# Performance work log

Hardware: AMD Instinct MI355X
Metric: run time of the kernel (lower is better)

The kernel has to match this reference:

```python
import jax, jax.numpy as jnp
import numpy as np

B, L, D_IN, D_MODEL, D_OUT, N_LAYERS, N2 = 16, 2048, 512, 512, 512, 4, 32
Q_STEP = 1.0 / 64.0
LN_EPS = 1e-5


def setup_inputs() -> dict:
    key = jax.random.key(0)
    ks = jax.random.split(key, 12)
    H = D_MODEL
    x = jax.random.normal(ks[0], (B, D_IN, L), jnp.float32)
    # sigma-delta dense encoder / decoder weights (ANN-equivalent: dense + ReLU)
    W_enc = jax.random.normal(ks[1], (H, D_IN), jnp.float32) * (1.0 / np.sqrt(D_IN))
    W_dec = jax.random.normal(ks[2], (D_OUT, H), jnp.float32) * (1.0 / np.sqrt(H))
    # S4D kernel params, stacked over layers. S4D-Lin init.
    log_dt = (jax.random.uniform(ks[3], (N_LAYERS, H), jnp.float32)
              * (np.log(0.1) - np.log(0.001)) + np.log(0.001))
    log_A_real = jnp.full((N_LAYERS, H, N2), np.log(0.5), jnp.float32)
    A_imag = jnp.tile((np.pi * jnp.arange(N2, dtype=jnp.float32))[None, None, :],
                      (N_LAYERS, H, 1))
    C_re = jax.random.normal(ks[4], (N_LAYERS, H, N2), jnp.float32) * (0.5 ** 0.5)
    C_im = jax.random.normal(ks[5], (N_LAYERS, H, N2), jnp.float32) * (0.5 ** 0.5)
    D = jax.random.normal(ks[6], (N_LAYERS, H), jnp.float32)
    # output linear of each S4D block: 1x1 conv H -> 2H followed by GLU
    W_out = jax.random.normal(ks[7], (N_LAYERS, 2 * H, H), jnp.float32) * (1.0 / np.sqrt(H))
    b_out = jnp.zeros((N_LAYERS, 2 * H), jnp.float32)
    ln_g = jnp.ones((N_LAYERS, H), jnp.float32)
    ln_b = jnp.zeros((N_LAYERS, H), jnp.float32)
    return {"x": x, "W_enc": W_enc, "W_dec": W_dec, "log_dt": log_dt,
            "log_A_real": log_A_real, "A_imag": A_imag, "C_re": C_re,
            "C_im": C_im, "D": D, "W_out": W_out, "b_out": b_out,
            "ln_g": ln_g, "ln_b": ln_b}


def _quantize_ste(x, step):
    q = jnp.round(x / step) * step
    return x + jax.lax.stop_gradient(q - x)


def reference(x, W_enc, W_dec, log_dt, log_A_real, A_imag, C_re, C_im, D,
              W_out, b_out, ln_g, ln_b):
    # x: (B, d_input, L) channel-time layout (slayer convention)
    xq = _quantize_ste(x, Q_STEP)
    h = jax.nn.relu(jnp.einsum('bct,dc->bdt', xq, W_enc))  # encoder (B,H,L)
    Lx = h.shape[-1]
    t = jnp.arange(Lx)
    for i in range(N_LAYERS):
        # ---- S4D kernel (ZOH-style discretization) ----
        dt = jnp.exp(log_dt[i])[:, None]                 # (H,1)
        A = -jnp.exp(log_A_real[i]) + 1j * A_imag[i]     # (H,N)
        dtA = dt * A                                     # (H,N)
        Cc = (C_re[i] + 1j * C_im[i]) * jnp.expm1(dtA) / A
        vand = jnp.exp(dtA[:, :, None] * t)              # (H,N,L)
        K = 2.0 * jnp.einsum('hn,hnl->hl', Cc, vand).real  # (H,L)
        # ---- FFT convolution ----
        k_f = jnp.fft.rfft(K, n=2 * Lx)                  # (H, L+1)
        u_f = jnp.fft.rfft(h, n=2 * Lx)                  # (B,H,L+1)
        y = jnp.fft.irfft(u_f * k_f[None], n=2 * Lx)[..., :Lx]
        y = y + D[i][:, None] * h                        # skip connection
        y = jax.nn.gelu(y, approximate=False)
        # output linear: 1x1 conv H->2H + GLU over channel dim
        z = jnp.einsum('bht,dh->bdt', y, W_out[i]) + b_out[i][None, :, None]
        z = z[:, :D_MODEL] * jax.nn.sigmoid(z[:, D_MODEL:])
        # residual + post-norm (LayerNorm over channel dim)
        h = z + h
        mu = h.mean(axis=1, keepdims=True)
        var = h.var(axis=1, keepdims=True)
        h = (h - mu) / jnp.sqrt(var + LN_EPS) * ln_g[i][:, None] + ln_b[i][:, None]
    out = jax.nn.relu(jnp.einsum('bht,dh->bdt', h, W_dec))  # decoder (B,d_out,L)
    return out
```

## Files before the change

### kernel.cpp

```cpp
#include <hip/hip_runtime.h>
#include <cstdint>
#include <cstddef>

typedef __attribute__((ext_vector_type(8))) short short8;
typedef __attribute__((ext_vector_type(8))) _Float16 half8;
typedef __attribute__((ext_vector_type(4))) float floatx4;
typedef __attribute__((ext_vector_type(4))) int intx4;
typedef __attribute__((ext_vector_type(4))) unsigned short ushort4v;

__device__ __forceinline__ unsigned short f2h(float f) {
    union { _Float16 h; unsigned short u; } v;
    v.h = (_Float16)f;
    return v.u;
}
__device__ __forceinline__ float relu_keepnan(float v) {
    return v > 0.f ? v : (v == v ? 0.f : v);
}

__global__ __launch_bounds__(256) void k_cvt(
    const float* __restrict__ src, unsigned short* __restrict__ dst, int n) {
    int i = blockIdx.x * 256 + threadIdx.x;
    if (i < n) dst[i] = f2h(src[i]);
}

__global__ __launch_bounds__(256) void k_precompute(
    const float* __restrict__ ldt, const float* __restrict__ lar,
    const float* __restrict__ aim, const float* __restrict__ cre,
    const float* __restrict__ cim, float4* __restrict__ lwc,
    float2* __restrict__ wt) {
    int idx = blockIdx.x * 256 + threadIdx.x;
    int i = idx >> 14;
    int h = (idx >> 5) & 511;
    int n = idx & 31;
    float dt = expf(ldt[i * 512 + h]);
    float Are = -expf(lar[idx]);
    float Aim = aim[idx];
    float dre = dt * Are, dim = dt * Aim;
    float e = expf(dre);
    float wre = e * cosf(dim);
    float wim = e * sinf(dim);
    float emr = wre - 1.f, emi = wim;
    float inv = 1.f / (Are * Are + Aim * Aim);
    float fr = (emr * Are + emi * Aim) * inv;
    float fi = (emi * Are - emr * Aim) * inv;
    float cr = cre[idx], ci = cim[idx];
    float4 o;
    o.x = wre; o.y = wim;
    o.z = 2.f * (cr * fr - ci * fi);
    o.w = 2.f * (cr * fi + ci * fr);
    int oidx = (i * 32 + n) * 512 + h;
    lwc[oidx] = o;
    float ar = wre, ai = wim;
#pragma unroll
    for (int k = 0; k < 7; ++k) {
        float nr = ar * ar - ai * ai;
        float ni = 2.f * ar * ai;
        ar = nr; ai = ni;
    }
    wt[oidx] = make_float2(ar, ai);
}

__global__ __launch_bounds__(256) void k_quant_transpose(
    const float* __restrict__ x, unsigned short* __restrict__ xq, int b0) {
    __shared__ unsigned short tile[64][65];
    const int bg = b0 + blockIdx.z, bl = blockIdx.z;
    const int c0 = blockIdx.y * 64, t0 = blockIdx.x * 64;
    const int tid = threadIdx.x;
#pragma unroll
    for (int it = 0; it < 16; ++it) {
        int idx = it * 256 + tid;
        int r = idx >> 6, cc = idx & 63;
        float f = x[(size_t)(bg * 512 + c0 + r) * 2048 + t0 + cc];
        float q = rintf(f * 64.f) * 0.015625f;
        tile[r][cc] = f2h(q);
    }
    __syncthreads();
#pragma unroll
    for (int it = 0; it < 16; ++it) {
        int idx = it * 256 + tid;
        int r = idx >> 6, cc = idx & 63;
        xq[(size_t)(bl * 2048 + t0 + r) * 512 + c0 + cc] = tile[cc][r];
    }
}

__global__ __launch_bounds__(256) void k_hf2ut(
    const float* __restrict__ hf, unsigned short* __restrict__ ut, int J) {
    __shared__ unsigned short tile[64][65];
    const int j0 = blockIdx.x * 64, c0 = blockIdx.y * 64;
    const int tid = threadIdx.x;
#pragma unroll
    for (int it = 0; it < 16; ++it) {
        int idx = it * 256 + tid;
        int r = idx >> 6, cc = idx & 63;
        tile[r][cc] = f2h(hf[(size_t)(j0 + r) * 512 + c0 + cc]);
    }
    __syncthreads();
#pragma unroll
    for (int it = 0; it < 16; ++it) {
        int idx = it * 256 + tid;
        int r = idx >> 6, cc = idx & 63;
        ut[(size_t)(c0 + r) * J + j0 + cc] = tile[cc][r];
    }
}

__global__ __launch_bounds__(64) void k_build_wa(
    const float4* __restrict__ lwc, unsigned short* __restrict__ WA, int layer) {
    __shared__ unsigned short Ws[64 * 136];
    const int h = blockIdx.x, tid = threadIdx.x;
    if (tid < 32) {
        float4 v = lwc[((size_t)layer * 32 + tid) * 512 + h];
        float pr = 1.f, pi = 0.f;
        for (int m = 0; m < 128; ++m) {
            Ws[(2 * tid) * 136 + (127 - m)] = f2h(pr);
            Ws[(2 * tid + 1) * 136 + (127 - m)] = f2h(pi);
            float nr = pr * v.x - pi * v.y;
            float ni = pr * v.y + pi * v.x;
            pr = nr; pi = ni;
        }
    }
    __syncthreads();
#pragma unroll
    for (int it = 0; it < 16; ++it) {
        int idx = it * 64 + tid;
        int r = idx >> 4, c8 = idx & 15;
        *(intx4*)(WA + (size_t)h * 8192 + r * 128 + c8 * 8) =
            *(const intx4*)(Ws + r * 136 + c8 * 8);
    }
}

__global__ __launch_bounds__(256) void k_build_T(
    const float4* __restrict__ lwc, const float* __restrict__ Dp,
    unsigned short* __restrict__ TT, int layer) {
    __shared__ float Kvs[128];
    __shared__ unsigned short Mxs[128 * 64];
    __shared__ float wr_s[32], wi_s[32], cr_s[32], ci_s[32];
    const int h = blockIdx.x, tid = threadIdx.x;
    if (tid < 32) {
        float4 v = lwc[((size_t)layer * 32 + tid) * 512 + h];
        wr_s[tid] = v.x; wi_s[tid] = v.y; cr_s[tid] = v.z; ci_s[tid] = v.w;
    }
    __syncthreads();
    if (tid < 32) {
        const int n = tid;
        float wre = wr_s[n], wim = wi_s[n];
        float ar = cr_s[n], ai = ci_s[n];
        for (int m = 0; m <= 128; ++m) {
            if (m < 128) {
                float s = ar;
#pragma unroll
                for (int d = 16; d >= 1; d >>= 1) s += __shfl_xor(s, d, 64);
                if (n == 0) Kvs[m] = s;
            }
            if (m >= 1) {
                Mxs[(m - 1) * 64 + 2 * n] = f2h(ar);
                Mxs[(m - 1) * 64 + 2 * n + 1] = f2h(-ai);
            }
            float nr = ar * wre - ai * wim;
            float ni = ar * wim + ai * wre;
            ar = nr; ai = ni;
        }
    }
    __syncthreads();
    const float Dh = Dp[layer * 512 + h];
#pragma unroll
    for (int it = 0; it < 12; ++it) {
        int idx = it * 256 + tid;
        int t = idx / 24, c8 = idx % 24;
        short8 pack;
#pragma unroll
        for (int q = 0; q < 8; ++q) {
            int k = c8 * 8 + q;
            unsigned short us;
            if (k < 128) {
                float val = (k <= t) ? (Kvs[t - k] + (k == t ? Dh : 0.f)) : 0.f;
                us = f2h(val);
            } else {
                us = Mxs[t * 64 + (k - 128)];
            }
            pack[q] = (short)us;
        }
        *(short8*)(TT + (size_t)h * 24576 + t * 192 + c8 * 8) = pack;
    }
}

template <int MODE>
__global__ __launch_bounds__(256, 2) void k_gemm(
    const unsigned short* __restrict__ A, const unsigned short* __restrict__ Bm,
    float* __restrict__ of32, int b0) {
    __shared__ __align__(16) unsigned short Al[128 * 72];
    __shared__ __align__(16) unsigned short Bl[128 * 72];
    const int tid = threadIdx.x;
    const int m0 = blockIdx.y * 128;
    const int j0 = blockIdx.x * 128;
    const int sub = tid & 7;
    const int row = tid >> 3;
    const unsigned short* Ag = A + (size_t)(m0 + row) * 512 + sub * 8;
    const unsigned short* Bg = Bm + (size_t)(j0 + row) * 512 + sub * 8;
    intx4 ra[4], rb[4];
#pragma unroll
    for (int i = 0; i < 4; ++i) {
        ra[i] = *(const intx4*)(Ag + (size_t)i * 32 * 512);
        rb[i] = *(const intx4*)(Bg + (size_t)i * 32 * 512);
    }
    const int lane = tid & 63;
    const int w = tid >> 6;
    const int wm = w & 1, wn = w >> 1;
    const int l15 = lane & 15, quad = lane >> 4;
    floatx4 acc[4][4] = {};
    for (int kt = 0; kt < 8; ++kt) {
#pragma unroll
        for (int i = 0; i < 4; ++i) {
            *(intx4*)(Al + (row + 32 * i) * 72 + sub * 8) = ra[i];
            *(intx4*)(Bl + (row + 32 * i) * 72 + sub * 8) = rb[i];
        }
        __syncthreads();
        if (kt < 7) {
#pragma unroll
            for (int i = 0; i < 4; ++i) {
                ra[i] = *(const intx4*)(Ag + (size_t)i * 32 * 512 + (kt + 1) * 64);
                rb[i] = *(const intx4*)(Bg + (size_t)i * 32 * 512 + (kt + 1) * 64);
            }
        }
#pragma unroll
        for (int ks = 0; ks < 2; ++ks) {
            half8 af[4], bfr[4];
#pragma unroll
            for (int mt = 0; mt < 4; ++mt)
                af[mt] = *(const half8*)(Al + (wm * 64 + mt * 16 + l15) * 72 + ks * 32 + quad * 8);
#pragma unroll
            for (int nt = 0; nt < 4; ++nt)
                bfr[nt] = *(const half8*)(Bl + (wn * 64 + nt * 16 + l15) * 72 + ks * 32 + quad * 8);
#pragma unroll
            for (int mt = 0; mt < 4; ++mt)
#pragma unroll
                for (int nt = 0; nt < 4; ++nt)
                    acc[mt][nt] = __builtin_amdgcn_mfma_f32_16x16x32_f16(
                        af[mt], bfr[nt], acc[mt][nt], 0, 0, 0);
        }
        __syncthreads();
    }
#pragma unroll
    for (int mt = 0; mt < 4; ++mt) {
#pragma unroll
        for (int nt = 0; nt < 4; ++nt) {
            const int d = m0 + wm * 64 + mt * 16 + quad * 4;
            const int j = j0 + wn * 64 + nt * 16 + l15;
            floatx4 v = acc[mt][nt];
            if (MODE == 0) {
#pragma unroll
                for (int r = 0; r < 4; ++r) v[r] = relu_keepnan(v[r]);
                *(floatx4*)(of32 + (size_t)j * 512 + d) = v;
            } else {
                const int bl = j >> 11, t = j & 2047;
#pragma unroll
                for (int r = 0; r < 4; ++r)
                    of32[((size_t)((b0 + bl) * 512 + d + r)) * 2048 + t] = relu_keepnan(v[r]);
            }
        }
    }
}

__global__ __launch_bounds__(256, 4) void k_stateA(
    const unsigned short* __restrict__ WA, const unsigned short* __restrict__ ut,
    float* __restrict__ P, int J, int Rtot) {
    __shared__ __align__(16) unsigned short Aw[64 * 72];
    __shared__ __align__(16) unsigned short Bw[128 * 72];
    const int tid = threadIdx.x;
    const int h = blockIdx.y;
    const int r0 = blockIdx.x * 128;
    const int sub = tid & 7, row = tid >> 3;
    const unsigned short* Ag = WA + (size_t)h * 8192 + row * 128 + sub * 8;
    const unsigned short* Bg = ut + (size_t)h * J + (size_t)(r0 + row) * 128 + sub * 8;
    intx4 ra[2], rb[4];
    ra[0] = *(const intx4*)(Ag);
    ra[1] = *(const intx4*)(Ag + 32 * 128);
#pragma unroll
    for (int i = 0; i < 4; ++i) rb[i] = *(const intx4*)(Bg + i * 32 * 128);
    const int lane = tid & 63, w = tid >> 6;
    const int wm = w & 1, wn = w >> 1;
    const int l15 = lane & 15, quad = lane >> 4;
    floatx4 acc[2][4] = {};
    for (int kt = 0; kt < 2; ++kt) {
        *(intx4*)(Aw + row * 72 + sub * 8) = ra[0];
        *(intx4*)(Aw + (row + 32) * 72 + sub * 8) = ra[1];
#pragma unroll
        for (int i = 0; i < 4; ++i)
            *(intx4*)(Bw + (row + 32 * i) * 72 + sub * 8) = rb[i];
        __syncthreads();
        if (kt == 0) {
            ra[0] = *(const intx4*)(Ag + 64);
            ra[1] = *(const intx4*)(Ag + 32 * 128 + 64);
#pragma unroll
            for (int i = 0; i < 4; ++i) rb[i] = *(const intx4*)(Bg + i * 32 * 128 + 64);
        }
#pragma unroll
        for (int ks = 0; ks < 2; ++ks) {
            half8 af[2], bfr[4];
#pragma unroll
            for (int mt = 0; mt < 2; ++mt)
                af[mt] = *(const half8*)(Aw + (wm * 32 + mt * 16 + l15) * 72 + ks * 32 + quad * 8);
#pragma unroll
            for (int nt = 0; nt < 4; ++nt)
                bfr[nt] = *(const half8*)(Bw + (wn * 64 + nt * 16 + l15) * 72 + ks * 32 + quad * 8);
#pragma unroll
            for (int mt = 0; mt < 2; ++mt)
#pragma unroll
                for (int nt = 0; nt < 4; ++nt)
                    acc[mt][nt] = __builtin_amdgcn_mfma_f32_16x16x32_f16(
                        af[mt], bfr[nt], acc[mt][nt], 0, 0, 0);
        }
        __syncthreads();
    }
#pragma unroll
    for (int mt = 0; mt < 2; ++mt)
#pragma unroll
        for (int nt = 0; nt < 4; ++nt)
#pragma unroll
            for (int r = 0; r < 4; ++r)
                P[((size_t)h * 64 + wm * 32 + mt * 16 + quad * 4 + r) * Rtot +
                  r0 + wn * 64 + nt * 16 + l15] = acc[mt][nt][r];
}

__global__ __launch_bounds__(64) void k_comb(
    const float* __restrict__ P, const float2* __restrict__ wt,
    unsigned short* __restrict__ S0, int layer, int Rtot) {
    __shared__ float Ps[64][17];
    __shared__ unsigned short S0s[16][64];
    const int h = blockIdx.x, bl = blockIdx.y;
    const int tid = threadIdx.x;
#pragma unroll
    for (int it = 0; it < 4; ++it) {
        int idx = it * 64 + tid;
        int n2 = idx >> 2, pt = idx & 3;
        float4 v = *(const float4*)(P + ((size_t)h * 64 + n2) * Rtot + bl * 16 + pt * 4);
        Ps[n2][pt * 4 + 0] = v.x; Ps[n2][pt * 4 + 1] = v.y;
        Ps[n2][pt * 4 + 2] = v.z; Ps[n2][pt * 4 + 3] = v.w;
    }
    __syncthreads();
    if (tid < 32) {
        const int n = tid;
        float2 wv = wt[((size_t)layer * 32 + n) * 512 + h];
        float ar = 0.f, ai = 0.f;
        for (int g = 0; g < 16; ++g) {
            S0s[g][2 * n] = f2h(ar);
            S0s[g][2 * n + 1] = f2h(ai);
            float pr = Ps[2 * n][g], pi = Ps[2 * n + 1][g];
            float nr = fmaf(wv.x, ar, fmaf(-wv.y, ai, pr));
            float ni = fmaf(wv.x, ai, fmaf(wv.y, ar, pi));
            ar = nr; ai = ni;
        }
    }
    __syncthreads();
    const int g = tid >> 2, pt = tid & 3;
    unsigned short* dst = S0 + ((size_t)h * Rtot + bl * 16 + g) * 64 + pt * 16;
    *(intx4*)(dst) = *(const intx4*)(&S0s[g][pt * 16]);
    *(intx4*)(dst + 8) = *(const intx4*)(&S0s[g][pt * 16 + 8]);
}

__global__ __launch_bounds__(256, 2) void k_applyB(
    const unsigned short* __restrict__ TT, const unsigned short* __restrict__ ut,
    const unsigned short* __restrict__ S0, unsigned short* __restrict__ vt,
    int J, int Rtot) {
    __shared__ __align__(16) unsigned short lds[2 * 128 * 72];
    unsigned short* Al = lds;
    unsigned short* Bl = lds + 128 * 72;
    const int tid = threadIdx.x;
    const int h = blockIdx.y;
    const int r0 = blockIdx.x * 128;
    const int sub = tid & 7, row = tid >> 3;
    const unsigned short* Ag = TT + (size_t)h * 24576 + row * 192 + sub * 8;
    const unsigned short* Bu = ut + (size_t)h * J + (size_t)(r0 + row) * 128 + sub * 8;
    const unsigned short* Bs = S0 + ((size_t)h * Rtot + r0 + row) * 64 + sub * 8;
    intx4 ra[4], rb[4];
#pragma unroll
    for (int i = 0; i < 4; ++i) {
        ra[i] = *(const intx4*)(Ag + i * 32 * 192);
        rb[i] = *(const intx4*)(Bu + i * 32 * 128);
    }
    const int lane = tid & 63, w = tid >> 6;
    const int wm = w & 1, wn = w >> 1;
    const int l15 = lane & 15, quad = lane >> 4;
    floatx4 acc[4][4] = {};
    for (int kt = 0; kt < 3; ++kt) {
#pragma unroll
        for (int i = 0; i < 4; ++i) {
            *(intx4*)(Al + (row + 32 * i) * 72 + sub * 8) = ra[i];
            *(intx4*)(Bl + (row + 32 * i) * 72 + sub * 8) = rb[i];
        }
        __syncthreads();
        if (kt == 0) {
#pragma unroll
            for (int i = 0; i < 4; ++i) {
                ra[i] = *(const intx4*)(Ag + i * 32 * 192 + 64);
                rb[i] = *(const intx4*)(Bu + i * 32 * 128 + 64);
            }
        } else if (kt == 1) {
#pragma unroll
            for (int i = 0; i < 4; ++i) {
                ra[i] = *(const intx4*)(Ag + i * 32 * 192 + 128);
                rb[i] = *(const intx4*)(Bs + i * 32 * 64);
            }
        }
#pragma unroll
        for (int ks = 0; ks < 2; ++ks) {
            half8 af[4], bfr[4];
#pragma unroll
            for (int mt = 0; mt < 4; ++mt)
                af[mt] = *(const half8*)(Al + (wm * 64 + mt * 16 + l15) * 72 + ks * 32 + quad * 8);
#pragma unroll
            for (int nt = 0; nt < 4; ++nt)
                bfr[nt] = *(const half8*)(Bl + (wn * 64 + nt * 16 + l15) * 72 + ks * 32 + quad * 8);
#pragma unroll
            for (int mt = 0; mt < 4; ++mt)
#pragma unroll
                for (int nt = 0; nt < 4; ++nt)
                    acc[mt][nt] = __builtin_amdgcn_mfma_f32_16x16x32_f16(
                        af[mt], bfr[nt], acc[mt][nt], 0, 0, 0);
        }
        __syncthreads();
    }
#pragma unroll
    for (int mt = 0; mt < 4; ++mt)
#pragma unroll
        for (int nt = 0; nt < 4; ++nt) {
            const int tl = wm * 64 + mt * 16 + quad * 4;
            const int rl = wn * 64 + nt * 16 + l15;
            ushort4v pack;
#pragma unroll
            for (int r = 0; r < 4; ++r) {
                float y = acc[mt][nt][r];
                float ge = 0.5f * y * (1.f + erff(y * 0.70710678118654752f));
                pack[r] = f2h(ge);
            }
            *(ushort4v*)(lds + rl * 136 + tl) = pack;
        }
    __syncthreads();
    const int rl2 = tid >> 1, hh = tid & 1;
    const unsigned short* srcp = lds + rl2 * 136 + hh * 64;
    unsigned short* dstp = vt + (size_t)h * J + (size_t)(r0 + rl2) * 128 + hh * 64;
#pragma unroll
    for (int q = 0; q < 8; ++q)
        *(intx4*)(dstp + q * 8) = *(const intx4*)(srcp + q * 8);
}

__global__ __launch_bounds__(256, 3) void k_gemm_glu(
    const unsigned short* __restrict__ A,
    const unsigned short* __restrict__ Bt,
    const float* __restrict__ bias,
    float* __restrict__ g_out, int J) {
    __shared__ __align__(16) unsigned short A1l[128 * 72];
    __shared__ __align__(16) unsigned short A2l[128 * 72];
    __shared__ __align__(16) unsigned short Bl[64 * 72];
    const int tid = threadIdx.x;
    const int m0 = blockIdx.y * 128;
    const int j0 = blockIdx.x * 64;
    const int sub = tid & 7;
    const int row = tid >> 3;
    const unsigned short* A1g = A + (size_t)(m0 + row) * 512 + sub * 8;
    const unsigned short* A2g = A1g + 512 * 512;
    const int chp = tid >> 3, jo = tid & 7;
    const unsigned short* Bg = Bt + (size_t)(2 * chp) * J + j0 + jo * 8;
    intx4 ra1[4], ra2[4], rb0, rb1;
#pragma unroll
    for (int i = 0; i < 4; ++i) {
        ra1[i] = *(const intx4*)(A1g + (size_t)i * 32 * 512);
        ra2[i] = *(const intx4*)(A2g + (size_t)i * 32 * 512);
    }
    rb0 = *(const intx4*)(Bg);
    rb1 = *(const intx4*)(Bg + J);
    const int lane = tid & 63;
    const int w = tid >> 6;
    const int wm = w & 1, wn = w >> 1;
    const int l15 = lane & 15, quad = lane >> 4;
    const int colbase = (((chp >> 2) ^ jo) << 3) + (chp & 3) * 2;
    floatx4 ac1[4][2] = {}, ac2[4][2] = {};
    for (int kt = 0; kt < 8; ++kt) {
#pragma unroll
        for (int i = 0; i < 4; ++i) {
            *(intx4*)(A1l + (row + 32 * i) * 72 + sub * 8) = ra1[i];
            *(intx4*)(A2l + (row + 32 * i) * 72 + sub * 8) = ra2[i];
        }
        {
            unsigned int* B32 = (unsigned int*)Bl;
#pragma unroll
            for (int i = 0; i < 4; ++i) {
                unsigned int ae = (unsigned int)rb0[i], be = (unsigned int)rb1[i];
                unsigned int lo = (ae & 0xffffu) | (be << 16);
                unsigned int hi = (ae >> 16) | (be & 0xffff0000u);
                B32[((jo * 8 + 2 * i) * 72 + colbase) >> 1] = lo;
                B32[((jo * 8 + 2 * i + 1) * 72 + colbase) >> 1] = hi;
            }
        }
        __syncthreads();
        if (kt < 7) {
#pragma unroll
            for (int i = 0; i < 4; ++i) {
                ra1[i] = *(const intx4*)(A1g + (size_t)i * 32 * 512 + (kt + 1) * 64);
                ra2[i] = *(const intx4*)(A2g + (size_t)i * 32 * 512 + (kt + 1) * 64);
            }
            rb0 = *(const intx4*)(Bg + (size_t)(kt + 1) * 64 * J);
            rb1 = *(const intx4*)(Bg + (size_t)(kt + 1) * 64 * J + J);
        }
#pragma unroll
        for (int ks = 0; ks < 2; ++ks) {
            half8 af1[4], af2[4], bfr[2];
#pragma unroll
            for (int mt = 0; mt < 4; ++mt) {
                af1[mt] = *(const half8*)(A1l + (wm * 64 + mt * 16 + l15) * 72 + ks * 32 + quad * 8);
                af2[mt] = *(const half8*)(A2l + (wm * 64 + mt * 16 + l15) * 72 + ks * 32 + quad * 8);
            }
#pragma unroll
            for (int nt = 0; nt < 2; ++nt) {
                const int rr = wn * 32 + nt * 16 + l15;
                const int cb = (ks * 4 + quad) ^ (rr >> 3);
                bfr[nt] = *(const half8*)(Bl + rr * 72 + cb * 8);
            }
#pragma unroll
            for (int mt = 0; mt < 4; ++mt)
#pragma unroll
                for (int nt = 0; nt < 2; ++nt) {
                    ac1[mt][nt] = __builtin_amdgcn_mfma_f32_16x16x32_f16(
                        af1[mt], bfr[nt], ac1[mt][nt], 0, 0, 0);
                    ac2[mt][nt] = __builtin_amdgcn_mfma_f32_16x16x32_f16(
                        af2[mt], bfr[nt], ac2[mt][nt], 0, 0, 0);
                }
        }
        __syncthreads();
    }
#pragma unroll
    for (int mt = 0; mt < 4; ++mt) {
#pragma unroll
        for (int nt = 0; nt < 2; ++nt) {
            const int d = m0 + wm * 64 + mt * 16 + quad * 4;
            const int j = j0 + wn * 32 + nt * 16 + l15;
            floatx4 v;
#pragma unroll
            for (int r = 0; r < 4; ++r) {
                float a = ac1[mt][nt][r] + bias[d + r];
                float gg = ac2[mt][nt][r] + bias[512 + d + r];
                v[r] = a / (1.f + expf(-gg));
            }
            *(floatx4*)(g_out + (size_t)j * 512 + d) = v;
        }
    }
}

__global__ __launch_bounds__(256, 4) void k_res_ln(
    const float* __restrict__ g, float* __restrict__ hf, unsigned short* __restrict__ hb,
    const float* __restrict__ lng, const float* __restrict__ lnb,
    int layer, int wh) {
    __shared__ float r1[4], r2[4];
    const size_t j = blockIdx.x;
    const float* gj = g + j * 512;
    float* hj = hf + j * 512;
    const int tid = threadIdx.x, lane = tid & 63, w = tid >> 6;
    float2 gv = *(const float2*)(gj + tid * 2);
    float2 hv = *(const float2*)(hj + tid * 2);
    float h0 = gv.x + hv.x, h1 = gv.y + hv.y;
    float s1 = h0 + h1, s2 = h0 * h0 + h1 * h1;
#pragma unroll
    for (int m = 32; m >= 1; m >>= 1) { s1 += __shfl_xor(s1, m, 64); s2 += __shfl_xor(s2, m, 64); }
    if (lane == 0) { r1[w] = s1; r2[w] = s2; }
    __syncthreads();
    const float S1 = r1[0] + r1[1] + r1[2] + r1[3];
    const float S2 = r2[0] + r2[1] + r2[2] + r2[3];
    const float mu = S1 * (1.f / 512.f);
    const float var = S2 * (1.f / 512.f) - mu * mu;
    const float isd = 1.f / sqrtf(var + 1e-5f);
    float2 gw = *(const float2*)(lng + layer * 512 + tid * 2);
    float2 bw = *(const float2*)(lnb + layer * 512 + tid * 2);
    float o0 = (h0 - mu) * isd * gw.x + bw.x;
    float o1 = (h1 - mu) * isd * gw.y + bw.y;
    *(float2*)(hj + tid * 2) = make_float2(o0, o1);
    if (wh) *(unsigned int*)(hb + j * 512 + tid * 2) =
        (unsigned int)f2h(o0) | ((unsigned int)f2h(o1) << 16);
}

extern "C" void kernel_launch(void* const* d_in, const int* in_sizes, int n_in,
                              void* d_out, int out_size, void* d_ws, size_t ws_size,
                              hipStream_t stream) {
    (void)in_sizes; (void)n_in; (void)out_size;
    const float* x      = (const float*)d_in[0];
    const float* W_enc  = (const float*)d_in[1];
    const float* W_dec  = (const float*)d_in[2];
    const float* log_dt = (const float*)d_in[3];
    const float* log_Ar = (const float*)d_in[4];
    const float* A_im   = (const float*)d_in[5];
    const float* C_re   = (const float*)d_in[6];
    const float* C_im   = (const float*)d_in[7];
    const float* Dp     = (const float*)d_in[8];
    const float* W_out  = (const float*)d_in[9];
    const float* b_out  = (const float*)d_in[10];
    const float* ln_g   = (const float*)d_in[11];
    const float* ln_b   = (const float*)d_in[12];

    int C = 16;
    while (C > 8 && (size_t)C * (12ull << 20) + (41ull << 20) > ws_size) C >>= 1;
    const size_t J = (size_t)C * 2048;
    const int Rtot = C * 16;

    char* ws = (char*)d_ws;
    size_t off = 0;
    auto alloc = [&](size_t bytes) { void* p = ws + off; off += (bytes + 255) & ~(size_t)255; return p; };
    float4*         lwc   = (float4*)alloc(4ull * 512 * 32 * 16);
    float2*         wt    = (float2*)alloc(4ull * 512 * 32 * 8);
    unsigned short* wencb = (unsigned short*)alloc(512 * 512 * 2);
    unsigned short* wdecb = (unsigned short*)alloc(512 * 512 * 2);
    unsigned short* woutb = (unsigned short*)alloc(4ull * 1024 * 512 * 2);
    unsigned short* WAb   = (unsigned short*)alloc(512ull * 64 * 128 * 2);
    unsigned short* TTb   = (unsigned short*)alloc(512ull * 128 * 192 * 2);
    unsigned short* ut    = (unsigned short*)alloc(512ull * J * 2);
    float*          g     = (float*)alloc(J * 512 * 4);
    float*          hf    = (float*)alloc(J * 512 * 4);
    unsigned short* vt    = (unsigned short*)alloc(J * 512 * 2);
    unsigned short* xq    = (unsigned short*)g;
    unsigned short* hb    = vt;
    float*          P     = (float*)g;
    unsigned short* S0u   = (unsigned short*)((char*)g + (size_t)C * (2ull << 20));

    k_precompute<<<256, 256, 0, stream>>>(log_dt, log_Ar, A_im, C_re, C_im, lwc, wt);
    k_cvt<<<1024, 256, 0, stream>>>(W_enc, wencb, 512 * 512);
    k_cvt<<<1024, 256, 0, stream>>>(W_dec, wdecb, 512 * 512);
    k_cvt<<<8192, 256, 0, stream>>>(W_out, woutb, 4 * 1024 * 512);
    for (int b0 = 0; b0 < 16; b0 += C) {
        k_quant_transpose<<<dim3(32, 8, C), 256, 0, stream>>>(x, xq, b0);
        k_gemm<0><<<dim3(C * 16, 4), 256, 0, stream>>>(wencb, xq, hf, 0);
        for (int i = 0; i < 4; ++i) {
            k_build_wa<<<512, 64, 0, stream>>>(lwc, WAb, i);
            k_build_T<<<512, 256, 0, stream>>>(lwc, Dp, TTb, i);
            k_hf2ut<<<dim3(C * 32, 8), 256, 0, stream>>>(hf, ut, (int)J);
            k_stateA<<<dim3(Rtot / 128, 512), 256, 0, stream>>>(WAb, ut, P, (int)J, Rtot);
            k_comb<<<dim3(512, C), 64, 0, stream>>>(P, wt, S0u, i, Rtot);
            k_applyB<<<dim3(Rtot / 128, 512), 256, 0, stream>>>(TTb, ut, S0u, vt, (int)J, Rtot);
            k_gemm_glu<<<dim3(C * 32, 4), 256, 0, stream>>>(
                woutb + (size_t)i * 1024 * 512, vt, b_out + (size_t)i * 1024, g, (int)J);
            k_res_ln<<<C * 2048, 256, 0, stream>>>(g, hf, hb, ln_g, ln_b, i, (i == 3) ? 1 : 0);
        }
        k_gemm<2><<<dim3(C * 16, 4), 256, 0, stream>>>(wdecb, hb, (float*)d_out, b0);
    }
}
```

Measured before the change: 1.057 ms.

## Fuse fp16 transpose into encoder GEMM and LayerNorm epilogues; widen GLU GEMM tile

Drops the standalone hf-to-ut transpose kernel. The encoder GEMM now writes the channel-major fp16 copy through LDS in its epilogue, and the LayerNorm kernel, which now handles 32 rows per block, writes the transposed fp16 tile for the next layer. This saves a full read of the fp32 activations and one kernel launch per layer. Separately, the GLU GEMM tile grows from 64 to 128 columns, which gives more reuse per block but lowers the occupancy hint from 3 to 2.

New measurement: 975.5 us. 1.08x faster.

```diff
diff --git a/kernel.cpp b/kernel.cpp
--- a/kernel.cpp
+++ b/kernel.cpp
@@ -83,26 +83,6 @@
     }
 }
 
-__global__ __launch_bounds__(256) void k_hf2ut(
-    const float* __restrict__ hf, unsigned short* __restrict__ ut, int J) {
-    __shared__ unsigned short tile[64][65];
-    const int j0 = blockIdx.x * 64, c0 = blockIdx.y * 64;
-    const int tid = threadIdx.x;
-#pragma unroll
-    for (int it = 0; it < 16; ++it) {
-        int idx = it * 256 + tid;
-        int r = idx >> 6, cc = idx & 63;
-        tile[r][cc] = f2h(hf[(size_t)(j0 + r) * 512 + c0 + cc]);
-    }
-    __syncthreads();
-#pragma unroll
-    for (int it = 0; it < 16; ++it) {
-        int idx = it * 256 + tid;
-        int r = idx >> 6, cc = idx & 63;
-        ut[(size_t)(c0 + r) * J + j0 + cc] = tile[cc][r];
-    }
-}
-
 __global__ __launch_bounds__(64) void k_build_wa(
     const float4* __restrict__ lwc, unsigned short* __restrict__ WA, int layer) {
     __shared__ unsigned short Ws[64 * 136];
@@ -186,9 +166,10 @@
 template <int MODE>
 __global__ __launch_bounds__(256, 2) void k_gemm(
     const unsigned short* __restrict__ A, const unsigned short* __restrict__ Bm,
-    float* __restrict__ of32, int b0) {
-    __shared__ __align__(16) unsigned short Al[128 * 72];
-    __shared__ __align__(16) unsigned short Bl[128 * 72];
+    float* __restrict__ of32, unsigned short* __restrict__ ut, int J, int b0) {
+    __shared__ __align__(16) unsigned short lds[2 * 128 * 72];
+    unsigned short* Al = lds;
+    unsigned short* Bl = lds + 128 * 72;
     const int tid = threadIdx.x;
     const int m0 = blockIdx.y * 128;
     const int j0 = blockIdx.x * 128;
@@ -243,20 +224,32 @@
     for (int mt = 0; mt < 4; ++mt) {
 #pragma unroll
         for (int nt = 0; nt < 4; ++nt) {
-            const int d = m0 + wm * 64 + mt * 16 + quad * 4;
-            const int j = j0 + wn * 64 + nt * 16 + l15;
+            const int dl = wm * 64 + mt * 16 + quad * 4;
+            const int jl = wn * 64 + nt * 16 + l15;
             floatx4 v = acc[mt][nt];
+#pragma unroll
+            for (int r = 0; r < 4; ++r) v[r] = relu_keepnan(v[r]);
             if (MODE == 0) {
-#pragma unroll
-                for (int r = 0; r < 4; ++r) v[r] = relu_keepnan(v[r]);
-                *(floatx4*)(of32 + (size_t)j * 512 + d) = v;
+                *(floatx4*)(of32 + (size_t)(j0 + jl) * 512 + m0 + dl) = v;
+#pragma unroll
+                for (int r = 0; r < 4; ++r) lds[(dl + r) * 136 + jl] = f2h(v[r]);
             } else {
+                const int j = j0 + jl;
                 const int bl = j >> 11, t = j & 2047;
 #pragma unroll
                 for (int r = 0; r < 4; ++r)
-                    of32[((size_t)((b0 + bl) * 512 + d + r)) * 2048 + t] = relu_keepnan(v[r]);
-            }
-        }
+                    of32[((size_t)((b0 + bl) * 512 + m0 + dl + r)) * 2048 + t] = v[r];
+            }
+        }
+    }
+    if (MODE == 0) {
+        __syncthreads();
+        const int drow = tid >> 1, hh = tid & 1;
+        const unsigned short* srcp = lds + drow * 136 + hh * 64;
+        unsigned short* dstp = ut + (size_t)(m0 + drow) * J + j0 + hh * 64;
+#pragma unroll
+        for (int q = 0; q < 8; ++q)
+            *(intx4*)(dstp + q * 8) = *(const intx4*)(srcp + q * 8);
     }
 }
 
@@ -443,37 +436,39 @@
         *(intx4*)(dstp + q * 8) = *(const intx4*)(srcp + q * 8);
 }
 
-__global__ __launch_bounds__(256, 3) void k_gemm_glu(
+__global__ __launch_bounds__(256, 2) void k_gemm_glu(
     const unsigned short* __restrict__ A,
     const unsigned short* __restrict__ Bt,
     const float* __restrict__ bias,
     float* __restrict__ g_out, int J) {
     __shared__ __align__(16) unsigned short A1l[128 * 72];
     __shared__ __align__(16) unsigned short A2l[128 * 72];
-    __shared__ __align__(16) unsigned short Bl[64 * 72];
+    __shared__ __align__(16) unsigned short Bl[128 * 72];
     const int tid = threadIdx.x;
     const int m0 = blockIdx.y * 128;
-    const int j0 = blockIdx.x * 64;
+    const int j0 = blockIdx.x * 128;
     const int sub = tid & 7;
     const int row = tid >> 3;
     const unsigned short* A1g = A + (size_t)(m0 + row) * 512 + sub * 8;
     const unsigned short* A2g = A1g + 512 * 512;
     const int chp = tid >> 3, jo = tid & 7;
     const unsigned short* Bg = Bt + (size_t)(2 * chp) * J + j0 + jo * 8;
-    intx4 ra1[4], ra2[4], rb0, rb1;
+    intx4 ra1[4], ra2[4], rb[4];
 #pragma unroll
     for (int i = 0; i < 4; ++i) {
         ra1[i] = *(const intx4*)(A1g + (size_t)i * 32 * 512);
         ra2[i] = *(const intx4*)(A2g + (size_t)i * 32 * 512);
     }
-    rb0 = *(const intx4*)(Bg);
-    rb1 = *(const intx4*)(Bg + J);
+    rb[0] = *(const intx4*)(Bg);
+    rb[1] = *(const intx4*)(Bg + J);
+    rb[2] = *(const intx4*)(Bg + 64);
+    rb[3] = *(const intx4*)(Bg + J + 64);
     const int lane = tid & 63;
     const int w = tid >> 6;
     const int wm = w & 1, wn = w >> 1;
     const int l15 = lane & 15, quad = lane >> 4;
     const int colbase = (((chp >> 2) ^ jo) << 3) + (chp & 3) * 2;
-    floatx4 ac1[4][2] = {}, ac2[4][2] = {};
+    floatx4 ac1[4][4] = {}, ac2[4][4] = {};
     for (int kt = 0; kt < 8; ++kt) {
 #pragma unroll
         for (int i = 0; i < 4; ++i) {
@@ -483,12 +478,17 @@
         {
             unsigned int* B32 = (unsigned int*)Bl;
 #pragma unroll
-            for (int i = 0; i < 4; ++i) {
-                unsigned int ae = (unsigned int)rb0[i], be = (unsigned int)rb1[i];
-                unsigned int lo = (ae & 0xffffu) | (be << 16);
-                unsigned int hi = (ae >> 16) | (be & 0xffff0000u);
-                B32[((jo * 8 + 2 * i) * 72 + colbase) >> 1] = lo;
-                B32[((jo * 8 + 2 * i + 1) * 72 + colbase) >> 1] = hi;
+            for (int half = 0; half < 2; ++half) {
+                const int jb = (jo + half * 8) * 8;
+                intx4 e0 = rb[half * 2], e1 = rb[half * 2 + 1];
+#pragma unroll
+                for (int i = 0; i < 4; ++i) {
+                    unsigned int ae = (unsigned int)e0[i], be = (unsigned int)e1[i];
+                    unsigned int lo = (ae & 0xffffu) | (be << 16);
+                    unsigned int hi = (ae >> 16) | (be & 0xffff0000u);
+                    B32[((jb + 2 * i) * 72 + colbase) >> 1] = lo;
+                    B32[((jb + 2 * i + 1) * 72 + colbase) >> 1] = hi;
+                }
             }
         }
         __syncthreads();
@@ -498,27 +498,29 @@
                 ra1[i] = *(const intx4*)(A1g + (size_t)i * 32 * 512 + (kt + 1) * 64);
                 ra2[i] = *(const intx4*)(A2g + (size_t)i * 32 * 512 + (kt + 1) * 64);
             }
-            rb0 = *(const intx4*)(Bg + (size_t)(kt + 1) * 64 * J);
-            rb1 = *(const intx4*)(Bg + (size_t)(kt + 1) * 64 * J + J);
+            rb[0] = *(const intx4*)(Bg + (size_t)(kt + 1) * 64 * J);
+            rb[1] = *(const intx4*)(Bg + (size_t)(kt + 1) * 64 * J + J);
+            rb[2] = *(const intx4*)(Bg + (size_t)(kt + 1) * 64 * J + 64);
+            rb[3] = *(const intx4*)(Bg + (size_t)(kt + 1) * 64 * J + J + 64);
         }
 #pragma unroll
         for (int ks = 0; ks < 2; ++ks) {
-            half8 af1[4], af2[4], bfr[2];
+            half8 af1[4], af2[4], bfr[4];
 #pragma unroll
             for (int mt = 0; mt < 4; ++mt) {
                 af1[mt] = *(const half8*)(A1l + (wm * 64 + mt * 16 + l15) * 72 + ks * 32 + quad * 8);
                 af2[mt] = *(const half8*)(A2l + (wm * 64 + mt * 16 + l15) * 72 + ks * 32 + quad * 8);
             }
 #pragma unroll
-            for (int nt = 0; nt < 2; ++nt) {
-                const int rr = wn * 32 + nt * 16 + l15;
-                const int cb = (ks * 4 + quad) ^ (rr >> 3);
+            for (int nt = 0; nt < 4; ++nt) {
+                const int rr = wn * 64 + nt * 16 + l15;
+                const int cb = (ks * 4 + quad) ^ ((rr >> 3) & 7);
                 bfr[nt] = *(const half8*)(Bl + rr * 72 + cb * 8);
             }
 #pragma unroll
             for (int mt = 0; mt < 4; ++mt)
 #pragma unroll
-                for (int nt = 0; nt < 2; ++nt) {
+                for (int nt = 0; nt < 4; ++nt) {
                     ac1[mt][nt] = __builtin_amdgcn_mfma_f32_16x16x32_f16(
                         af1[mt], bfr[nt], ac1[mt][nt], 0, 0, 0);
                     ac2[mt][nt] = __builtin_amdgcn_mfma_f32_16x16x32_f16(
@@ -530,9 +532,9 @@
 #pragma unroll
     for (int mt = 0; mt < 4; ++mt) {
 #pragma unroll
-        for (int nt = 0; nt < 2; ++nt) {
+        for (int nt = 0; nt < 4; ++nt) {
             const int d = m0 + wm * 64 + mt * 16 + quad * 4;
-            const int j = j0 + wn * 32 + nt * 16 + l15;
+            const int j = j0 + wn * 64 + nt * 16 + l15;
             floatx4 v;
 #pragma unroll
             for (int r = 0; r < 4; ++r) {
@@ -545,35 +547,67 @@
     }
 }
 
-__global__ __launch_bounds__(256, 4) void k_res_ln(
-    const float* __restrict__ g, float* __restrict__ hf, unsigned short* __restrict__ hb,
+__global__ __launch_bounds__(256, 4) void k_res_ln_t(
+    const float* __restrict__ g, float* __restrict__ hf,
+    unsigned short* __restrict__ ut, unsigned short* __restrict__ hb,
     const float* __restrict__ lng, const float* __restrict__ lnb,
-    int layer, int wh) {
-    __shared__ float r1[4], r2[4];
-    const size_t j = blockIdx.x;
+    int layer, int J, int mode) {
+    __shared__ unsigned short tile[64 * 40];
+    const int tid = threadIdx.x;
+    const int r = tid >> 3, sub = tid & 7;
+    const int j0 = blockIdx.x * 32;
+    const size_t j = (size_t)j0 + r;
     const float* gj = g + j * 512;
     float* hj = hf + j * 512;
-    const int tid = threadIdx.x, lane = tid & 63, w = tid >> 6;
-    float2 gv = *(const float2*)(gj + tid * 2);
-    float2 hv = *(const float2*)(hj + tid * 2);
-    float h0 = gv.x + hv.x, h1 = gv.y + hv.y;
-    float s1 = h0 + h1, s2 = h0 * h0 + h1 * h1;
-#pragma unroll
-    for (int m = 32; m >= 1; m >>= 1) { s1 += __shfl_xor(s1, m, 64); s2 += __shfl_xor(s2, m, 64); }
-    if (lane == 0) { r1[w] = s1; r2[w] = s2; }
-    __syncthreads();
-    const float S1 = r1[0] + r1[1] + r1[2] + r1[3];
-    const float S2 = r2[0] + r2[1] + r2[2] + r2[3];
-    const float mu = S1 * (1.f / 512.f);
-    const float var = S2 * (1.f / 512.f) - mu * mu;
+    floatx4 v[16];
+    float s1 = 0.f, s2 = 0.f;
+#pragma unroll
+    for (int k = 0; k < 16; ++k) {
+        floatx4 gv = *(const floatx4*)(gj + sub * 4 + k * 32);
+        floatx4 hv = *(const floatx4*)(hj + sub * 4 + k * 32);
+        floatx4 vv = gv + hv;
+        v[k] = vv;
+        s1 += vv[0] + vv[1] + vv[2] + vv[3];
+        s2 += vv[0] * vv[0] + vv[1] * vv[1] + vv[2] * vv[2] + vv[3] * vv[3];
+    }
+#pragma unroll
+    for (int m = 4; m >= 1; m >>= 1) { s1 += __shfl_xor(s1, m, 64); s2 += __shfl_xor(s2, m, 64); }
+    const float mu = s1 * (1.f / 512.f);
+    const float var = s2 * (1.f / 512.f) - mu * mu;
     const float isd = 1.f / sqrtf(var + 1e-5f);
-    float2 gw = *(const float2*)(lng + layer * 512 + tid * 2);
-    float2 bw = *(const float2*)(lnb + layer * 512 + tid * 2);
-    float o0 = (h0 - mu) * isd * gw.x + bw.x;
-    float o1 = (h1 - mu) * isd * gw.y + bw.y;
-    *(float2*)(hj + tid * 2) = make_float2(o0, o1);
-    if (wh) *(unsigned int*)(hb + j * 512 + tid * 2) =
-        (unsigned int)f2h(o0) | ((unsigned int)f2h(o1) << 16);
+#pragma unroll
+    for (int t = 0; t < 8; ++t) {
+        if (mode == 1 && t) __syncthreads();
+#pragma unroll
+        for (int kk = 0; kk < 2; ++kk) {
+            const int k = t * 2 + kk;
+            const int cho = sub * 4 + k * 32;
+            floatx4 gw = *(const floatx4*)(lng + layer * 512 + cho);
+            floatx4 bw = *(const floatx4*)(lnb + layer * 512 + cho);
+            floatx4 o;
+#pragma unroll
+            for (int i = 0; i < 4; ++i) o[i] = (v[k][i] - mu) * isd * gw[i] + bw[i];
+            *(floatx4*)(hj + cho) = o;
+            if (mode == 1) {
+                const int chl = kk * 32 + sub * 4;
+#pragma unroll
+                for (int i = 0; i < 4; ++i)
+                    tile[(chl + i) * 40 + (r ^ ((((chl + i) >> 2) & 3) << 3))] = f2h(o[i]);
+            } else {
+                ushort4v p;
+#pragma unroll
+                for (int i = 0; i < 4; ++i) p[i] = f2h(o[i]);
+                *(ushort4v*)(hb + j * 512 + cho) = p;
+            }
+        }
+        if (mode == 1) {
+            __syncthreads();
+            const int chrow = tid >> 2, part = tid & 3;
+            const int pb = part ^ ((chrow >> 2) & 3);
+            *(intx4*)(ut + (size_t)(t * 64 + chrow) * J + j0 + part * 8) =
+                *(const intx4*)(tile + chrow * 40 + pb * 8);
+        }
+    }
 }
 
 extern "C" void kernel_launch(void* const* d_in, const int* in_sizes, int n_in,
@@ -624,18 +658,18 @@
     k_cvt<<<8192, 256, 0, stream>>>(W_out, woutb, 4 * 1024 * 512);
     for (int b0 = 0; b0 < 16; b0 += C) {
         k_quant_transpose<<<dim3(32, 8, C), 256, 0, stream>>>(x, xq, b0);
-        k_gemm<0><<<dim3(C * 16, 4), 256, 0, stream>>>(wencb, xq, hf, 0);
+        k_gemm<0><<<dim3(C * 16, 4), 256, 0, stream>>>(wencb, xq, hf, ut, (int)J, 0);
         for (int i = 0; i < 4; ++i) {
             k_build_wa<<<512, 64, 0, stream>>>(lwc, WAb, i);
             k_build_T<<<512, 256, 0, stream>>>(lwc, Dp, TTb, i);
-            k_hf2ut<<<dim3(C * 32, 8), 256, 0, stream>>>(hf, ut, (int)J);
             k_stateA<<<dim3(Rtot / 128, 512), 256, 0, stream>>>(WAb, ut, P, (int)J, Rtot);
             k_comb<<<dim3(512, C), 64, 0, stream>>>(P, wt, S0u, i, Rtot);
             k_applyB<<<dim3(Rtot / 128, 512), 256, 0, stream>>>(TTb, ut, S0u, vt, (int)J, Rtot);
-            k_gemm_glu<<<dim3(C * 32, 4), 256, 0, stream>>>(
+            k_gemm_glu<<<dim3(C * 16, 4), 256, 0, stream>>>(
                 woutb + (size_t)i * 1024 * 512, vt, b_out + (size_t)i * 1024, g, (int)J);
-            k_res_ln<<<C * 2048, 256, 0, stream>>>(g, hf, hb, ln_g, ln_b, i, (i == 3) ? 1 : 0);
-        }
-        k_gemm<2><<<dim3(C * 16, 4), 256, 0, stream>>>(wdecb, hb, (float*)d_out, b0);
-    }
-}
+            k_res_ln_t<<<(int)(J / 32), 256, 0, stream>>>(
+                g, hf, ut, hb, ln_g, ln_b, i, (int)J, (i == 3) ? 2 : 1);
+        }
+        k_gemm<2><<<dim3(C * 16, 4), 256, 0, stream>>>(wdecb, hb, (float*)d_out, nullptr, 0, b0);
+    }
+}
```
